# Optimization experiments

Hardware: AMD Instinct MI355X
Metric: run time of the kernel (lower is better)

## Reference

```python
import jax, jax.numpy as jnp
import numpy as np

NODE_DIM = 128
EDGE_DIM = 128
N_NODES = 10000
N_EDGES = 640000


def setup_inputs() -> dict:
    key = jax.random.key(0)
    ks = jax.random.split(key, 11)
    x = jax.random.normal(ks[0], (N_NODES, NODE_DIM), dtype=jnp.float32)
    edge_index = jax.random.randint(ks[1], (2, N_EDGES), 0, N_NODES, dtype=jnp.int32)
    edge_attr = jax.random.normal(ks[2], (N_EDGES, EDGE_DIM), dtype=jnp.float32)

    def lin(k, fan_in, fan_out):
        kw, kb = jax.random.split(k)
        bound = 1.0 / np.sqrt(fan_in)
        W = jax.random.uniform(kw, (fan_in, fan_out), minval=-bound, maxval=bound, dtype=jnp.float32)
        b = jax.random.uniform(kb, (fan_out,), minval=-bound, maxval=bound, dtype=jnp.float32)
        return W, b

    # node_update: Linear(node+edge -> node), Softplus, Linear(node -> node)
    nW1, nb1 = lin(ks[3], NODE_DIM + EDGE_DIM, NODE_DIM)
    nW2, nb2 = lin(ks[4], NODE_DIM, NODE_DIM)
    # edge_update_net: Linear(2*node+edge -> edge), Softplus, Linear(edge -> edge)
    eW1, eb1 = lin(ks[5], 2 * NODE_DIM + EDGE_DIM, EDGE_DIM)
    eW2, eb2 = lin(ks[6], EDGE_DIM, EDGE_DIM)

    return {
        "x": x, "edge_index": edge_index, "edge_attr": edge_attr,
        "nW1": nW1, "nb1": nb1, "nW2": nW2, "nb2": nb2,
        "eW1": eW1, "eb1": eb1, "eW2": eW2, "eb2": eb2,
    }


def reference(x, edge_index, edge_attr, nW1, nb1, nW2, nb2, eW1, eb1, eW2, eb2):
    row, col = edge_index[0], edge_index[1]
    x_row = x[row]              # [E, node_dim]
    x_col = x[col]              # [E, node_dim]

    # edge update MLP
    edge_input = jnp.concatenate([x_row, x_col, edge_attr], axis=1)  # [E, 2n+e]
    h = jax.nn.softplus(edge_input @ eW1 + eb1)
    edge_attr_new = h @ eW2 + eb2                                     # [E, edge_dim]

    # node message MLP
    msg_in = jnp.concatenate([x_row, edge_attr_new], axis=1)          # [E, n+e]
    m = jax.nn.softplus(msg_in @ nW1 + nb1)
    messages = m @ nW2 + nb2                                          # [E, node_dim]

    # scatter_add messages into destination nodes (col)
    x_new = jax.ops.segment_sum(messages, col, num_segments=x.shape[0])
    return (x_new, edge_attr_new)
```

## Files before the change

kernel.cpp:

```cpp
#include <hip/hip_runtime.h>
#include <cstdint>

#define N_NODES   10000
#define N_EDGES   640000
#define NODE_OUT  (N_NODES * 128)

typedef __bf16 bf16;
typedef bf16  bf16x8 __attribute__((ext_vector_type(8)));
typedef float f32x4  __attribute__((ext_vector_type(4)));

#define EW1T_OFF 0
#define EW2T_OFF 49152
#define NW1T_OFF 65536
#define NW2T_OFF 98304

__global__ void transpose_weights(const float* __restrict__ eW1, const float* __restrict__ eW2,
                                  const float* __restrict__ nW1, const float* __restrict__ nW2,
                                  bf16* __restrict__ wt) {
  int gid = blockIdx.x * 256 + threadIdx.x;
  const float* src; bf16* dst; int K, off;
  if (gid < 49152)      { src = eW1; dst = wt + EW1T_OFF; K = 384; off = gid; }
  else if (gid < 65536) { src = eW2; dst = wt + EW2T_OFF; K = 128; off = gid - 49152; }
  else if (gid < 98304) { src = nW1; dst = wt + NW1T_OFF; K = 256; off = gid - 65536; }
  else                  { src = nW2; dst = wt + NW2T_OFF; K = 128; off = gid - 98304; }
  int k = off >> 7, n = off & 127;
  dst[n * K + k] = (bf16)src[off];
}

__device__ __forceinline__ float softplus_f(float v) {
  return v > 20.f ? v : __logf(1.f + __expf(v));
}

__device__ __forceinline__ bf16x8 load_cvt8(const float* __restrict__ src) {
  float4 f0 = *(const float4*)src;
  float4 f1 = *(const float4*)(src + 4);
  bf16x8 h;
  h[0] = (bf16)f0.x; h[1] = (bf16)f0.y; h[2] = (bf16)f0.z; h[3] = (bf16)f0.w;
  h[4] = (bf16)f1.x; h[5] = (bf16)f1.y; h[6] = (bf16)f1.z; h[7] = (bf16)f1.w;
  return h;
}

template <int K, int SLOT_BASE>
__device__ __forceinline__ void run_gemm(const bf16* __restrict__ WT,
                                         const bf16* sA, bf16* sB,
                                         int wave, int lane, int m0, int n0,
                                         f32x4 (&acc)[2][4]) {
  const int ln15 = lane & 15, lq = lane >> 4;
  constexpr int NC = K >> 5;
  const int r0 = m0 + ln15, r1 = r0 + 16;
  const int sw = ln15 & 7;
  #pragma unroll
  for (int tm = 0; tm < 2; ++tm)
    #pragma unroll
    for (int tn = 0; tn < 4; ++tn)
      acc[tm][tn] = f32x4{0.f, 0.f, 0.f, 0.f};

  const bf16* wsrc = WT + (wave * 16 + ln15) * K + lq * 8;
  uint4 pre = *(const uint4*)wsrc;
  const int bslot = (wave * 64 + lane) * 8;
  const int tb = n0 >> 4;

  #pragma unroll
  for (int c = 0; c < NC; ++c) {
    bf16* buf = sB + (c & 1) * 4096;
    *(uint4*)&buf[bslot] = pre;
    if (c + 1 < NC) pre = *(const uint4*)(wsrc + (c + 1) * 32);
    __syncthreads();
    const int ls = SLOT_BASE + (c << 2) + lq;
    bf16x8 a0 = *(const bf16x8*)&sA[r0 * 384 + ((ls ^ sw) << 3)];
    bf16x8 a1 = *(const bf16x8*)&sA[r1 * 384 + ((ls ^ sw) << 3)];
    #pragma unroll
    for (int tn = 0; tn < 4; ++tn) {
      bf16x8 b = *(const bf16x8*)&buf[((tb + tn) * 64 + lane) * 8];
      acc[0][tn] = __builtin_amdgcn_mfma_f32_16x16x32_bf16(a0, b, acc[0][tn], 0, 0, 0);
      acc[1][tn] = __builtin_amdgcn_mfma_f32_16x16x32_bf16(a1, b, acc[1][tn], 0, 0, 0);
    }
  }
  __syncthreads();
}

__global__ void __launch_bounds__(512, 2)
fused_mpnn(const float* __restrict__ x, const int* __restrict__ eidx,
           const float* __restrict__ edge_attr,
           const float* __restrict__ eb1, const float* __restrict__ eb2,
           const float* __restrict__ nb1, const float* __restrict__ nb2,
           const bf16* __restrict__ wt,
           float* __restrict__ node_out, float* __restrict__ edge_out)
{
  extern __shared__ char smem[];
  bf16* sA = (bf16*)smem;
  bf16* sB = (bf16*)(smem + 98304);

  const int tid  = threadIdx.x;
  const int wave = tid >> 6, lane = tid & 63;
  const int ln15 = lane & 15, lq = lane >> 4;
  const int m0 = (wave >> 1) * 32;
  const int n0 = (wave & 1) * 64;
  const int e0 = blockIdx.x * 128;

  #pragma unroll
  for (int it = 0; it < 12; ++it) {
    int j  = it * 512 + tid;
    int region = j >> 11;
    int jj = j & 2047;
    int e  = jj >> 4, pl = jj & 15;
    int lp = pl ^ (e & 7);
    const float* src;
    if (region == 0)      src = x + (size_t)eidx[e0 + e] * 128 + lp * 8;
    else if (region == 1) src = x + (size_t)eidx[N_EDGES + e0 + e] * 128 + lp * 8;
    else                  src = edge_attr + (size_t)(e0 + e) * 128 + lp * 8;
    *(bf16x8*)&sA[e * 384 + ((region << 4) + pl) * 8] = load_cvt8(src);
  }

  f32x4 acc[2][4];

  run_gemm<384, 0>(wt + EW1T_OFF, sA, sB, wave, lane, m0, n0, acc);
  {
    float bias[4];
    #pragma unroll
    for (int tn = 0; tn < 4; ++tn) bias[tn] = eb1[n0 + tn * 16 + ln15];
    #pragma unroll
    for (int tm = 0; tm < 2; ++tm)
      #pragma unroll
      for (int tn = 0; tn < 4; ++tn)
        #pragma unroll
        for (int r = 0; r < 4; ++r) {
          float v = softplus_f(acc[tm][tn][r] + bias[tn]);
          int row = m0 + tm * 16 + lq * 4 + r;
          int col = n0 + tn * 16 + ln15;
          int ls  = 32 + (col >> 3);
          sA[row * 384 + ((ls ^ (row & 7)) << 3) + (col & 7)] = (bf16)v;
        }
  }

  run_gemm<128, 32>(wt + EW2T_OFF, sA, sB, wave, lane, m0, n0, acc);
  {
    float bias[4];
    #pragma unroll
    for (int tn = 0; tn < 4; ++tn) bias[tn] = eb2[n0 + tn * 16 + ln15];
    #pragma unroll
    for (int tm = 0; tm < 2; ++tm)
      #pragma unroll
      for (int tn = 0; tn < 4; ++tn)
        #pragma unroll
        for (int r = 0; r < 4; ++r) {
          float v = acc[tm][tn][r] + bias[tn];
          int row = m0 + tm * 16 + lq * 4 + r;
          int col = n0 + tn * 16 + ln15;
          edge_out[(size_t)(e0 + row) * 128 + col] = v;
          int ls = 16 + (col >> 3);
          sA[row * 384 + ((ls ^ (row & 7)) << 3) + (col & 7)] = (bf16)v;
        }
  }

  run_gemm<256, 0>(wt + NW1T_OFF, sA, sB, wave, lane, m0, n0, acc);
  {
    float bias[4];
    #pragma unroll
    for (int tn = 0; tn < 4; ++tn) bias[tn] = nb1[n0 + tn * 16 + ln15];
    #pragma unroll
    for (int tm = 0; tm < 2; ++tm)
      #pragma unroll
      for (int tn = 0; tn < 4; ++tn)
        #pragma unroll
        for (int r = 0; r < 4; ++r) {
          float v = softplus_f(acc[tm][tn][r] + bias[tn]);
          int row = m0 + tm * 16 + lq * 4 + r;
          int col = n0 + tn * 16 + ln15;
          int ls  = 32 + (col >> 3);
          sA[row * 384 + ((ls ^ (row & 7)) << 3) + (col & 7)] = (bf16)v;
        }
  }

  run_gemm<128, 32>(wt + NW2T_OFF, sA, sB, wave, lane, m0, n0, acc);
  {
    float bias[4];
    #pragma unroll
    for (int tn = 0; tn < 4; ++tn) bias[tn] = nb2[n0 + tn * 16 + ln15];
    #pragma unroll
    for (int tm = 0; tm < 2; ++tm) {
      int nodes[4];
      #pragma unroll
      for (int r = 0; r < 4; ++r)
        nodes[r] = eidx[N_EDGES + e0 + m0 + tm * 16 + lq * 4 + r];
      #pragma unroll
      for (int tn = 0; tn < 4; ++tn) {
        int col = n0 + tn * 16 + ln15;
        #pragma unroll
        for (int r = 0; r < 4; ++r) {
          float v = acc[tm][tn][r] + bias[tn];
          unsafeAtomicAdd(&node_out[(size_t)nodes[r] * 128 + col], v);
        }
      }
    }
  }
}

extern "C" void kernel_launch(void* const* d_in, const int* in_sizes, int n_in,
                              void* d_out, int out_size, void* d_ws, size_t ws_size,
                              hipStream_t stream) {
  const float* x    = (const float*)d_in[0];
  const int*   eidx = (const int*)d_in[1];
  const float* ea   = (const float*)d_in[2];
  const float* nW1  = (const float*)d_in[3];
  const float* nb1  = (const float*)d_in[4];
  const float* nW2  = (const float*)d_in[5];
  const float* nb2  = (const float*)d_in[6];
  const float* eW1  = (const float*)d_in[7];
  const float* eb1  = (const float*)d_in[8];
  const float* eW2  = (const float*)d_in[9];
  const float* eb2  = (const float*)d_in[10];

  bf16*  wt        = (bf16*)d_ws;
  float* out_nodes = (float*)d_out;
  float* out_edges = out_nodes + NODE_OUT;

  hipMemsetAsync(out_nodes, 0, NODE_OUT * sizeof(float), stream);
  transpose_weights<<<448, 256, 0, stream>>>(eW1, eW2, nW1, nW2, wt);
  fused_mpnn<<<N_EDGES / 128, 512, 98304 + 16384, stream>>>(
      x, eidx, ea, eb1, eb2, nb1, nb2, wt, out_nodes, out_edges);
}
```

Measured before the change: 1.014 ms.

## Read weight fragments directly from global memory and halve block tile to 64 edges

Removes the shared-memory staging of weight tiles and the per-chunk barriers, so each wave loads its B fragments straight from global (L2-cached) transposed weights. The block shrinks to 256 threads handling 64 edges with 48KB LDS, which allows more resident blocks per CU and fewer barriers. The trade-off is redundant global and L2 weight traffic, since every wave fetches its own weight fragments each chunk without reuse through LDS.

```diff
diff --git a/kernel.cpp b/kernel.cpp
--- a/kernel.cpp
+++ b/kernel.cpp
@@ -42,8 +42,8 @@
 
 template <int K, int SLOT_BASE>
 __device__ __forceinline__ void run_gemm(const bf16* __restrict__ WT,
-                                         const bf16* sA, bf16* sB,
-                                         int wave, int lane, int m0, int n0,
+                                         const bf16* sA,
+                                         int lane, int m0, int n0,
                                          f32x4 (&acc)[2][4]) {
   const int ln15 = lane & 15, lq = lane >> 4;
   constexpr int NC = K >> 5;
@@ -55,31 +55,23 @@
     for (int tn = 0; tn < 4; ++tn)
       acc[tm][tn] = f32x4{0.f, 0.f, 0.f, 0.f};
 
-  const bf16* wsrc = WT + (wave * 16 + ln15) * K + lq * 8;
-  uint4 pre = *(const uint4*)wsrc;
-  const int bslot = (wave * 64 + lane) * 8;
-  const int tb = n0 >> 4;
+  const bf16* bbase = WT + (size_t)(n0 + ln15) * K + lq * 8;
 
   #pragma unroll
   for (int c = 0; c < NC; ++c) {
-    bf16* buf = sB + (c & 1) * 4096;
-    *(uint4*)&buf[bslot] = pre;
-    if (c + 1 < NC) pre = *(const uint4*)(wsrc + (c + 1) * 32);
-    __syncthreads();
     const int ls = SLOT_BASE + (c << 2) + lq;
     bf16x8 a0 = *(const bf16x8*)&sA[r0 * 384 + ((ls ^ sw) << 3)];
     bf16x8 a1 = *(const bf16x8*)&sA[r1 * 384 + ((ls ^ sw) << 3)];
     #pragma unroll
     for (int tn = 0; tn < 4; ++tn) {
-      bf16x8 b = *(const bf16x8*)&buf[((tb + tn) * 64 + lane) * 8];
+      bf16x8 b = *(const bf16x8*)(bbase + tn * 16 * K + (c << 5));
       acc[0][tn] = __builtin_amdgcn_mfma_f32_16x16x32_bf16(a0, b, acc[0][tn], 0, 0, 0);
       acc[1][tn] = __builtin_amdgcn_mfma_f32_16x16x32_bf16(a1, b, acc[1][tn], 0, 0, 0);
     }
   }
-  __syncthreads();
-}
-
-__global__ void __launch_bounds__(512, 2)
+}
+
+__global__ void __launch_bounds__(256, 3)
 fused_mpnn(const float* __restrict__ x, const int* __restrict__ eidx,
            const float* __restrict__ edge_attr,
            const float* __restrict__ eb1, const float* __restrict__ eb2,
@@ -89,20 +81,19 @@
 {
   extern __shared__ char smem[];
   bf16* sA = (bf16*)smem;
-  bf16* sB = (bf16*)(smem + 98304);
 
   const int tid  = threadIdx.x;
   const int wave = tid >> 6, lane = tid & 63;
   const int ln15 = lane & 15, lq = lane >> 4;
   const int m0 = (wave >> 1) * 32;
   const int n0 = (wave & 1) * 64;
-  const int e0 = blockIdx.x * 128;
+  const int e0 = blockIdx.x * 64;
 
   #pragma unroll
   for (int it = 0; it < 12; ++it) {
-    int j  = it * 512 + tid;
-    int region = j >> 11;
-    int jj = j & 2047;
+    int j  = it * 256 + tid;
+    int region = j >> 10;
+    int jj = j & 1023;
     int e  = jj >> 4, pl = jj & 15;
     int lp = pl ^ (e & 7);
     const float* src;
@@ -111,10 +102,12 @@
     else                  src = edge_attr + (size_t)(e0 + e) * 128 + lp * 8;
     *(bf16x8*)&sA[e * 384 + ((region << 4) + pl) * 8] = load_cvt8(src);
   }
+  __syncthreads();
 
   f32x4 acc[2][4];
 
-  run_gemm<384, 0>(wt + EW1T_OFF, sA, sB, wave, lane, m0, n0, acc);
+  run_gemm<384, 0>(wt + EW1T_OFF, sA, lane, m0, n0, acc);
+  __syncthreads();
   {
     float bias[4];
     #pragma unroll
@@ -132,8 +125,10 @@
           sA[row * 384 + ((ls ^ (row & 7)) << 3) + (col & 7)] = (bf16)v;
         }
   }
-
-  run_gemm<128, 32>(wt + EW2T_OFF, sA, sB, wave, lane, m0, n0, acc);
+  __syncthreads();
+
+  run_gemm<128, 32>(wt + EW2T_OFF, sA, lane, m0, n0, acc);
+  __syncthreads();
   {
     float bias[4];
     #pragma unroll
@@ -152,8 +147,10 @@
           sA[row * 384 + ((ls ^ (row & 7)) << 3) + (col & 7)] = (bf16)v;
         }
   }
-
-  run_gemm<256, 0>(wt + NW1T_OFF, sA, sB, wave, lane, m0, n0, acc);
+  __syncthreads();
+
+  run_gemm<256, 0>(wt + NW1T_OFF, sA, lane, m0, n0, acc);
+  __syncthreads();
   {
     float bias[4];
     #pragma unroll
@@ -171,8 +168,9 @@
           sA[row * 384 + ((ls ^ (row & 7)) << 3) + (col & 7)] = (bf16)v;
         }
   }
-
-  run_gemm<128, 32>(wt + NW2T_OFF, sA, sB, wave, lane, m0, n0, acc);
+  __syncthreads();
+
+  run_gemm<128, 32>(wt + NW2T_OFF, sA, lane, m0, n0, acc);
   {
     float bias[4];
     #pragma unroll
@@ -217,6 +215,6 @@
 
   hipMemsetAsync(out_nodes, 0, NODE_OUT * sizeof(float), stream);
   transpose_weights<<<448, 256, 0, stream>>>(eW1, eW2, nW1, nW2, wt);
-  fused_mpnn<<<N_EDGES / 128, 512, 98304 + 16384, stream>>>(
+  fused_mpnn<<<N_EDGES / 64, 256, 49152, stream>>>(
       x, eidx, ea, eb1, eb2, nb1, nb2, wt, out_nodes, out_edges);
 }
```

Measured after the change: 1.090 ms. +7.5%, slower.
